# Optimization experiments

Hardware: AMD Instinct MI355X
Metric: run time of the kernel (lower is better)

## Reference

```python
import jax, jax.numpy as jnp
import numpy as np

B, N_COLS, N_PROMPTS, D = 1024, 256, 128, 256


def _ln(x, g, b, eps=1e-5):
    m = jnp.mean(x, axis=-1, keepdims=True)
    v = jnp.mean(jnp.square(x - m), axis=-1, keepdims=True)
    return (x - m) * jax.lax.rsqrt(v + eps) * g + b


def setup_inputs() -> dict:
    key = jax.random.key(0)
    ks = jax.random.split(key, 10)
    d_rs = D ** -0.5
    return {
        "x": jax.random.normal(ks[0], (B, N_COLS), jnp.float32),
        "prev_cell_out": jax.random.normal(ks[1], (B, N_PROMPTS, D), jnp.float32),
        "feature_emb_weight": jax.random.uniform(ks[2], (N_COLS, D), jnp.float32, -d_rs, d_rs),
        "feature_emb_bias": jax.random.uniform(ks[3], (N_COLS, D), jnp.float32, -d_rs, d_rs),
        "ln_emb_g": jnp.ones((D,), jnp.float32),
        "ln_emb_b": jnp.zeros((D,), jnp.float32),
        "ln_col_g": jnp.ones((D,), jnp.float32),
        "ln_col_b": jnp.zeros((D,), jnp.float32),
        "ln_prompt_g": jnp.ones((D,), jnp.float32),
        "ln_prompt_b": jnp.zeros((D,), jnp.float32),
        # torch Linear(2*D, D): weight [D, 2*D], y = x @ W^T + b
        "dense_imp_w": jax.random.normal(ks[4], (D, 2 * D), jnp.float32) * (2 * D) ** -0.5,
        "dense_imp_b": jnp.zeros((D,), jnp.float32),
        "emb_column": jax.random.normal(ks[5], (N_COLS, D), jnp.float32) * 0.01,
        "emb_prompt": jax.random.normal(ks[6], (N_PROMPTS, D), jnp.float32) * 0.01,
        # dense_expand = Linear(1, n_prompts): weight [n_prompts,1] squeezed -> [n_prompts]
        "expand_w": jax.random.normal(ks[7], (N_PROMPTS,), jnp.float32),
        "expand_b": jax.random.normal(ks[8], (N_PROMPTS,), jnp.float32) * 0.01,
    }


def reference(x, prev_cell_out, feature_emb_weight, feature_emb_bias,
              ln_emb_g, ln_emb_b, ln_col_g, ln_col_b, ln_prompt_g, ln_prompt_b,
              dense_imp_w, dense_imp_b, emb_column, emb_prompt,
              expand_w, expand_b):
    # feature embedding: [B, N, D]
    x_emb = jax.nn.relu(jnp.einsum('bn,nd->bnd', x, feature_emb_weight) + feature_emb_bias)
    x_emb = _ln(x_emb, ln_emb_g, ln_emb_b)
    # prompt update with residual
    xp = jnp.broadcast_to(emb_prompt[None], (x.shape[0], N_PROMPTS, D))  # [B, P, D]
    cat = jnp.concatenate([_ln(xp, ln_prompt_g, ln_prompt_b), prev_cell_out], axis=-1)  # [B, P, 2D]
    xp = jnp.einsum('bpk,dk->bpd', cat, dense_imp_w) + dense_imp_b + xp
    # column keys (shared across batch)
    col = _ln(emb_column, ln_col_g, ln_col_b)  # [N, D]
    mask = jax.nn.softmax(jnp.einsum('bpd,nd->bpn', xp, col), axis=-1)  # [B, P, N]
    V = jnp.einsum('bpn,bnd->bpd', mask, x_emb)  # [B, P, D]
    return V * (1.0 + expand_w)[None, :, None] + expand_b[None, :, None]
```

## Files before the change

kernel.cpp:

```cpp
#include <hip/hip_runtime.h>

#define NCOLS 256
#define NP    128
#define DD    256

typedef _Float16 half2 __attribute__((ext_vector_type(2)));
typedef _Float16 half4 __attribute__((ext_vector_type(4)));
typedef float    f32x4 __attribute__((ext_vector_type(4)));

#define MFMA16(a,b,c) __builtin_amdgcn_mfma_f32_16x16x16f16(a,b,c,0,0,0)

#define WS_COL_LN   0
#define WS_LNP      262144
#define WS_BASE     393216
#define WS_BLOG     524288
#define WS_CW16     655360
#define WS_WB16     786432

#define SMEM_LOGIT 67584
#define SMEM_PV    34816


__global__ __launch_bounds__(256) void k0a(
    const float* __restrict__ emb_column, const float* __restrict__ emb_prompt,
    const float* __restrict__ ln_col_g, const float* __restrict__ ln_col_b,
    const float* __restrict__ ln_prompt_g, const float* __restrict__ ln_prompt_b,
    const float* __restrict__ few, const float* __restrict__ feb,
    char* __restrict__ ws)
{
    __shared__ float red[10];
    int blk = blockIdx.x, tid = threadIdx.x;
    if (blk < 384) {
        const float *src, *g, *bb; float* dst;
        if (blk < 256) { int r = blk;     src = emb_column + r*DD; g = ln_col_g;    bb = ln_col_b;    dst = (float*)(ws + WS_COL_LN) + r*DD; }
        else           { int r = blk-256; src = emb_prompt + r*DD; g = ln_prompt_g; bb = ln_prompt_b; dst = (float*)(ws + WS_LNP) + r*DD; }
        float v = src[tid];
        float s = v, q = v*v;
        #pragma unroll
        for (int off = 32; off; off >>= 1) { s += __shfl_xor(s, off); q += __shfl_xor(q, off); }
        int wid = tid >> 6, lane = tid & 63;
        if (lane == 0) { red[wid] = s; red[4+wid] = q; }
        __syncthreads();
        if (tid == 0) {
            float S = red[0]+red[1]+red[2]+red[3];
            float Q = red[4]+red[5]+red[6]+red[7];
            float mu = S * (1.0f/DD);
            float var = Q * (1.0f/DD) - mu*mu;
            red[8] = mu; red[9] = rsqrtf(var + 1e-5f);
        }
        __syncthreads();
        dst[tid] = (v - red[8]) * red[9] * g[tid] + bb[tid];
    } else {
        int base = (blk - 384) * 512;
        half2* wb = (half2*)(ws + WS_WB16);
        #pragma unroll
        for (int j = 0; j < 2; ++j) {
            int idx = base + j*256 + tid;
            half2 h; h[0] = (_Float16)few[idx]; h[1] = (_Float16)feb[idx];
            wb[idx] = h;
        }
    }
}

__global__ __launch_bounds__(256) void k0b(
    const float* __restrict__ diw, const float* __restrict__ dib,
    const float* __restrict__ emb_prompt, char* __restrict__ ws)
{
    __shared__ float rowv[DD];
    int blk = blockIdx.x, tid = threadIdx.x;
    if (blk < 256) {
        int n = blk;
        const float* col_ln = (const float*)(ws + WS_COL_LN);
        rowv[tid] = col_ln[n*DD + tid];
        __syncthreads();
        float acc = 0.f;
        #pragma unroll 4
        for (int d = 0; d < DD; ++d) acc += rowv[d] * diw[d*512 + 256 + tid];
        int nt = n >> 4, lr = n & 15;
        int kc = tid >> 4, lq = (tid >> 2) & 3, j = tid & 3;
        ((_Float16*)(ws + WS_CW16))[((kc*16 + nt)*64 + lq*16 + lr)*4 + j] = (_Float16)acc;
    } else {
        int p = blk - 256;
        const float* lnp = (const float*)(ws + WS_LNP);
        rowv[tid] = lnp[p*DD + tid];
        __syncthreads();
        float acc = 0.f;
        #pragma unroll 4
        for (int k = 0; k < DD; ++k) acc += rowv[k] * diw[tid*512 + k];
        ((float*)(ws + WS_BASE))[p*DD + tid] = acc + dib[tid] + emb_prompt[p*DD + tid];
    }
}

__global__ __launch_bounds__(256) void k0c(char* __restrict__ ws)
{
    __shared__ float bs[DD];
    int p = blockIdx.x, n = threadIdx.x;
    const float* base   = (const float*)(ws + WS_BASE);
    const float* col_ln = (const float*)(ws + WS_COL_LN);
    bs[n] = base[p*DD + n];
    __syncthreads();
    float acc = 0.f;
    #pragma unroll 4
    for (int d = 0; d < DD; ++d) acc += bs[d] * col_ln[n*DD + d];
    ((float*)(ws + WS_BLOG))[p*DD + n] = acc;
}

__global__ __launch_bounds__(512, 4) void k_logit(
    const float* __restrict__ prev, const char* __restrict__ ws,
    char* __restrict__ pbuf)
{
    extern __shared__ char smem[];
    float* sm_m = (float*)(smem + 65536);
    float* sm_l = (float*)(smem + 66560);

    const char* cwbase = ws + WS_CW16;

    int bid = blockIdx.x;
    int b = bid >> 1, ph = bid & 1;
    int tid = threadIdx.x;
    int w = tid >> 6, l = tid & 63, lq = l >> 4, lr = l & 15;
    int pt = w >> 1, nh = w & 1;
    int pl = 16*pt + lr;
    int p  = 64*ph + pl;

    half4 pfrag[16];
    {
        const float* prow = prev + ((size_t)b*NP + p)*DD + 4*lq;
        #pragma unroll
        for (int kc = 0; kc < 16; ++kc) {
            f32x4 v = *(const f32x4*)(prow + 16*kc);
            half4 h;
            #pragma unroll
            for (int j = 0; j < 4; ++j) h[j] = (_Float16)v[j];
            pfrag[kc] = h;
        }
    }

    auto stage_cw = [&](int c, char* dst) {
        #pragma unroll
        for (int i = 0; i < 4; ++i) {
            int u = tid + 512*i;
            int kc = u >> 7, ntg = (u >> 5) & 3, rem = u & 31;
            uint4 v = *(const uint4*)(cwbase + kc*8192 + c*2048 + ntg*512 + rem*16);
            *(uint4*)(dst + u*16) = v;
        }
    };

    f32x4 acc[8];
    {
        const float* blrow = (const float*)(ws + WS_BLOG) + (size_t)p*DD + 4*lq;
        #pragma unroll
        for (int a = 0; a < 8; ++a)
            acc[a] = *(const f32x4*)(blrow + 16*(4*(a>>1) + 2*nh + (a&1)));
    }

    stage_cw(0, smem);
    __syncthreads();

    #pragma unroll
    for (int c = 0; c < 4; ++c) {
        char* cwc = smem + ((c & 1) ? 32768 : 0);
        char* cwn = smem + ((c & 1) ? 0 : 32768);

        uint4 st[4];
        if (c < 3) {
            #pragma unroll
            for (int i = 0; i < 4; ++i) {
                int u = tid + 512*i;
                int kc = u >> 7, ntg = (u >> 5) & 3, rem = u & 31;
                st[i] = *(const uint4*)(cwbase + kc*8192 + (c+1)*2048 + ntg*512 + rem*16);
            }
        }

        const char* cwl = cwc + l*8 + nh*1024;
        #pragma unroll
        for (int kc = 0; kc < 16; ++kc) {
            const char* fb = cwl + kc*2048;
            half4 a0 = *(const half4*)(fb);
            half4 a1 = *(const half4*)(fb + 512);
            half4 bp = pfrag[kc];
            acc[2*c]   = MFMA16(a0, bp, acc[2*c]);
            acc[2*c+1] = MFMA16(a1, bp, acc[2*c+1]);
        }

        if (c < 3) {
            #pragma unroll
            for (int i = 0; i < 4; ++i) {
                int u = tid + 512*i;
                *(uint4*)(cwn + u*16) = st[i];
            }
        }
        __syncthreads();
    }

    float pmax = -1e30f;
    #pragma unroll
    for (int a = 0; a < 8; ++a)
        #pragma unroll
        for (int r = 0; r < 4; ++r) pmax = fmaxf(pmax, acc[a][r]);
    pmax = fmaxf(pmax, __shfl_xor(pmax, 16));
    pmax = fmaxf(pmax, __shfl_xor(pmax, 32));
    if (lq == 0) sm_m[nh*64 + pl] = pmax;
    __syncthreads();
    float m = fmaxf(pmax, sm_m[(1 ^ nh)*64 + pl]);

    float s = 0.f;
    #pragma unroll
    for (int a = 0; a < 8; ++a)
        #pragma unroll
        for (int r = 0; r < 4; ++r) { float e = __expf(acc[a][r] - m); acc[a][r] = e; s += e; }
    s += __shfl_xor(s, 16);
    s += __shfl_xor(s, 32);
    if (lq == 0) sm_l[nh*64 + pl] = s;
    __syncthreads();
    float inv = 1.0f / (s + sm_l[(1 ^ nh)*64 + pl]);

    char* Pb = pbuf + (size_t)b*131072;
    #pragma unroll
    for (int a = 0; a < 8; ++a) {
        int NT = 4*(a >> 1) + 2*nh + (a & 1);
        half4 h;
        #pragma unroll
        for (int r = 0; r < 4; ++r) h[r] = (_Float16)(acc[a][r] * inv);
        *(half4*)(Pb + p*512 + NT*32 + lq*8) = h;
    }
}

__global__ __launch_bounds__(512, 4) void k_pv(
    const float* __restrict__ x,
    const float* __restrict__ expand_w, const float* __restrict__ expand_b,
    const float* __restrict__ ln_emb_g, const float* __restrict__ ln_emb_b,
    const char* __restrict__ ws, float* __restrict__ out)
{
    extern __shared__ char smem[];
    float* x_s = (float*)smem;
    char* xe0 = smem + 2048;
    char* xe1 = smem + 18432;

    const half2* WB = (const half2*)(ws + WS_WB16);

    int b = blockIdx.x;
    int tid = threadIdx.x;
    int w = tid >> 6, l = tid & 63, lq = l >> 4, lr = l & 15;
    int p = 16*w + lr;

    if (tid < 256) x_s[tid] = x[b*NCOLS + tid];
    float gcc[4], bcc[4];
    #pragma unroll
    for (int cc = 0; cc < 4; ++cc) {
        gcc[cc] = ln_emb_g[l + 64*cc];
        bcc[cc] = ln_emb_b[l + 64*cc];
    }

    const char* Pb = (const char*)out + (size_t)b*131072;

    auto compute_xe = [&](int c, char* xebuf) {
        int kc2 = w >> 2, lq2 = w & 3;
        float vj[4][4];
        #pragma unroll
        for (int j = 0; j < 4; ++j) {
            int n = c*32 + 16*kc2 + 4*lq2 + j;
            float xv = x_s[n];
            const half2* wbrow = WB + n*DD;
            float s = 0.f, q = 0.f;
            #pragma unroll
            for (int cc = 0; cc < 4; ++cc) {
                half2 pp = wbrow[l + 64*cc];
                float e = fmaf(xv, (float)pp[0], (float)pp[1]);
                e = e > 0.f ? e : 0.f;
                vj[j][cc] = e; s += e; q += e*e;
            }
            #pragma unroll
            for (int off = 32; off; off >>= 1) { s += __shfl_xor(s, off); q += __shfl_xor(q, off); }
            float mu = s * (1.0f/DD);
            float rs = rsqrtf(q*(1.0f/DD) - mu*mu + 1e-5f);
            #pragma unroll
            for (int cc = 0; cc < 4; ++cc)
                vj[j][cc] = (vj[j][cc]-mu)*rs*gcc[cc] + bcc[cc];
        }
        #pragma unroll
        for (int cc = 0; cc < 4; ++cc) {
            int dt = 4*cc + (l >> 4);
            half4 h;
            #pragma unroll
            for (int j = 0; j < 4; ++j) h[j] = (_Float16)vj[j][cc];
            *(half4*)(xebuf + (((kc2*16 + dt)*64) + lq2*16 + lr)*8) = h;
        }
    };

    __syncthreads();
    compute_xe(0, xe0);

    f32x4 acc_v[16];
    #pragma unroll
    for (int dt = 0; dt < 16; ++dt) acc_v[dt] = (f32x4){0.f,0.f,0.f,0.f};

    __syncthreads();

    for (int c = 0; c < 8; ++c) {
        char* xec = (c & 1) ? xe1 : xe0;
        char* xen = (c & 1) ? xe0 : xe1;

        half4 p16c[2];
        #pragma unroll
        for (int kc2 = 0; kc2 < 2; ++kc2)
            p16c[kc2] = *(const half4*)(Pb + p*512 + c*64 + kc2*32 + lq*8);

        if (c < 7) compute_xe(c+1, xen);

        const char* xel = xec + l*8;
        #pragma unroll
        for (int kc2 = 0; kc2 < 2; ++kc2) {
            half4 bp = p16c[kc2];
            const char* xb = xel + kc2*8192;
            #pragma unroll
            for (int dt = 0; dt < 16; ++dt) {
                half4 a = *(const half4*)(xb + dt*512);
                acc_v[dt] = MFMA16(a, bp, acc_v[dt]);
            }
        }

        __syncthreads();
    }

    {
        float sw = 1.0f + expand_w[p];
        float sb = expand_b[p];
        float* orow = out + ((size_t)b*NP + p)*DD + 4*lq;
        #pragma unroll
        for (int dt = 0; dt < 16; ++dt) {
            f32x4 v = acc_v[dt];
            #pragma unroll
            for (int r = 0; r < 4; ++r) v[r] = v[r]*sw + sb;
            *(f32x4*)(orow + 16*dt) = v;
        }
    }
}

extern "C" void kernel_launch(void* const* d_in, const int* in_sizes, int n_in,
                              void* d_out, int out_size, void* d_ws, size_t ws_size,
                              hipStream_t stream) {
    (void)in_sizes; (void)n_in; (void)out_size; (void)ws_size;
    const float* x           = (const float*)d_in[0];
    const float* prev        = (const float*)d_in[1];
    const float* few         = (const float*)d_in[2];
    const float* feb         = (const float*)d_in[3];
    const float* ln_emb_g    = (const float*)d_in[4];
    const float* ln_emb_b    = (const float*)d_in[5];
    const float* ln_col_g    = (const float*)d_in[6];
    const float* ln_col_b    = (const float*)d_in[7];
    const float* ln_prompt_g = (const float*)d_in[8];
    const float* ln_prompt_b = (const float*)d_in[9];
    const float* diw         = (const float*)d_in[10];
    const float* dib         = (const float*)d_in[11];
    const float* emb_column  = (const float*)d_in[12];
    const float* emb_prompt  = (const float*)d_in[13];
    const float* expand_w    = (const float*)d_in[14];
    const float* expand_b    = (const float*)d_in[15];
    char* ws = (char*)d_ws;
    float* out = (float*)d_out;

    k0a<<<512, 256, 0, stream>>>(emb_column, emb_prompt, ln_col_g, ln_col_b,
                                 ln_prompt_g, ln_prompt_b, few, feb, ws);
    k0b<<<384, 256, 0, stream>>>(diw, dib, emb_prompt, ws);
    k0c<<<128, 256, 0, stream>>>(ws);

    (void)hipFuncSetAttribute(reinterpret_cast<const void*>(k_logit),
                              hipFuncAttributeMaxDynamicSharedMemorySize, SMEM_LOGIT);
    k_logit<<<2048, 512, SMEM_LOGIT, stream>>>(prev, ws, (char*)d_out);

    (void)hipFuncSetAttribute(reinterpret_cast<const void*>(k_pv),
                              hipFuncAttributeMaxDynamicSharedMemorySize, SMEM_PV);
    k_pv<<<1024, 512, SMEM_PV, stream>>>(x, expand_w, expand_b,
                                         ln_emb_g, ln_emb_b, ws, out);
}
```

Measured before the change: 218.9 us.

## Fuse logit-softmax and PV kernels into one per-batch kernel with LDS-resident probabilities

Merges the logit/softmax kernel and the P·V kernel into a single 1024-thread block per batch element. The softmax probabilities stay in LDS with an XOR swizzle, so the fp16 P matrix no longer makes a round trip through global memory (the output buffer). The whole fp16 column-weight matrix is staged into LDS at once instead of being double-buffered in chunks. Each wave pair now splits the output D dimension, and the x_emb chunks are larger. The cost is about 131KB of LDS per block, which limits occupancy to roughly one block per CU, and fewer waves are available to hide latency.

```diff
diff --git a/kernel.cpp b/kernel.cpp
--- a/kernel.cpp
+++ b/kernel.cpp
@@ -17,8 +17,10 @@
 #define WS_CW16     655360
 #define WS_WB16     786432
 
-#define SMEM_LOGIT 67584
-#define SMEM_PV    34816
+#define LDS_CWP   3072
+#define LDS_XE0   68608
+#define LDS_XE1   101376
+#define SMEM_MAIN 134144
 
 
 __global__ __launch_bounds__(256) void k0a(
@@ -105,146 +107,103 @@
     ((float*)(ws + WS_BLOG))[p*DD + n] = acc;
 }
 
-__global__ __launch_bounds__(512, 4) void k_logit(
-    const float* __restrict__ prev, const char* __restrict__ ws,
-    char* __restrict__ pbuf)
-{
-    extern __shared__ char smem[];
-    float* sm_m = (float*)(smem + 65536);
-    float* sm_l = (float*)(smem + 66560);
-
-    const char* cwbase = ws + WS_CW16;
-
-    int bid = blockIdx.x;
-    int b = bid >> 1, ph = bid & 1;
-    int tid = threadIdx.x;
-    int w = tid >> 6, l = tid & 63, lq = l >> 4, lr = l & 15;
-    int pt = w >> 1, nh = w & 1;
-    int pl = 16*pt + lr;
-    int p  = 64*ph + pl;
-
-    half4 pfrag[16];
-    {
-        const float* prow = prev + ((size_t)b*NP + p)*DD + 4*lq;
-        #pragma unroll
-        for (int kc = 0; kc < 16; ++kc) {
-            f32x4 v = *(const f32x4*)(prow + 16*kc);
-            half4 h;
-            #pragma unroll
-            for (int j = 0; j < 4; ++j) h[j] = (_Float16)v[j];
-            pfrag[kc] = h;
-        }
-    }
-
-    auto stage_cw = [&](int c, char* dst) {
-        #pragma unroll
-        for (int i = 0; i < 4; ++i) {
-            int u = tid + 512*i;
-            int kc = u >> 7, ntg = (u >> 5) & 3, rem = u & 31;
-            uint4 v = *(const uint4*)(cwbase + kc*8192 + c*2048 + ntg*512 + rem*16);
-            *(uint4*)(dst + u*16) = v;
-        }
-    };
-
-    f32x4 acc[8];
-    {
-        const float* blrow = (const float*)(ws + WS_BLOG) + (size_t)p*DD + 4*lq;
-        #pragma unroll
-        for (int a = 0; a < 8; ++a)
-            acc[a] = *(const f32x4*)(blrow + 16*(4*(a>>1) + 2*nh + (a&1)));
-    }
-
-    stage_cw(0, smem);
-    __syncthreads();
-
-    #pragma unroll
-    for (int c = 0; c < 4; ++c) {
-        char* cwc = smem + ((c & 1) ? 32768 : 0);
-        char* cwn = smem + ((c & 1) ? 0 : 32768);
-
-        uint4 st[4];
-        if (c < 3) {
-            #pragma unroll
-            for (int i = 0; i < 4; ++i) {
-                int u = tid + 512*i;
-                int kc = u >> 7, ntg = (u >> 5) & 3, rem = u & 31;
-                st[i] = *(const uint4*)(cwbase + kc*8192 + (c+1)*2048 + ntg*512 + rem*16);
-            }
-        }
-
-        const char* cwl = cwc + l*8 + nh*1024;
-        #pragma unroll
-        for (int kc = 0; kc < 16; ++kc) {
-            const char* fb = cwl + kc*2048;
-            half4 a0 = *(const half4*)(fb);
-            half4 a1 = *(const half4*)(fb + 512);
-            half4 bp = pfrag[kc];
-            acc[2*c]   = MFMA16(a0, bp, acc[2*c]);
-            acc[2*c+1] = MFMA16(a1, bp, acc[2*c+1]);
-        }
-
-        if (c < 3) {
-            #pragma unroll
-            for (int i = 0; i < 4; ++i) {
-                int u = tid + 512*i;
-                *(uint4*)(cwn + u*16) = st[i];
-            }
-        }
-        __syncthreads();
-    }
-
-    float pmax = -1e30f;
-    #pragma unroll
-    for (int a = 0; a < 8; ++a)
-        #pragma unroll
-        for (int r = 0; r < 4; ++r) pmax = fmaxf(pmax, acc[a][r]);
-    pmax = fmaxf(pmax, __shfl_xor(pmax, 16));
-    pmax = fmaxf(pmax, __shfl_xor(pmax, 32));
-    if (lq == 0) sm_m[nh*64 + pl] = pmax;
-    __syncthreads();
-    float m = fmaxf(pmax, sm_m[(1 ^ nh)*64 + pl]);
-
-    float s = 0.f;
-    #pragma unroll
-    for (int a = 0; a < 8; ++a)
-        #pragma unroll
-        for (int r = 0; r < 4; ++r) { float e = __expf(acc[a][r] - m); acc[a][r] = e; s += e; }
-    s += __shfl_xor(s, 16);
-    s += __shfl_xor(s, 32);
-    if (lq == 0) sm_l[nh*64 + pl] = s;
-    __syncthreads();
-    float inv = 1.0f / (s + sm_l[(1 ^ nh)*64 + pl]);
-
-    char* Pb = pbuf + (size_t)b*131072;
-    #pragma unroll
-    for (int a = 0; a < 8; ++a) {
-        int NT = 4*(a >> 1) + 2*nh + (a & 1);
-        half4 h;
-        #pragma unroll
-        for (int r = 0; r < 4; ++r) h[r] = (_Float16)(acc[a][r] * inv);
-        *(half4*)(Pb + p*512 + NT*32 + lq*8) = h;
-    }
-}
-
-__global__ __launch_bounds__(512, 4) void k_pv(
-    const float* __restrict__ x,
+__global__ __launch_bounds__(1024) void trompt_main(
+    const float* __restrict__ x, const float* __restrict__ prev,
     const float* __restrict__ expand_w, const float* __restrict__ expand_b,
     const float* __restrict__ ln_emb_g, const float* __restrict__ ln_emb_b,
     const char* __restrict__ ws, float* __restrict__ out)
 {
     extern __shared__ char smem[];
-    float* x_s = (float*)smem;
-    char* xe0 = smem + 2048;
-    char* xe1 = smem + 18432;
-
-    const half2* WB = (const half2*)(ws + WS_WB16);
+    float* x_s  = (float*)(smem);
+    float* sm_m = (float*)(smem + 1024);
+    float* sm_l = (float*)(smem + 2048);
+    char*  cwP  = smem + LDS_CWP;
+    char*  xe0  = smem + LDS_XE0;
+    char*  xe1  = smem + LDS_XE1;
+
+    const char*  cwbase = ws + WS_CW16;
+    const half2* WB     = (const half2*)(ws + WS_WB16);
 
     int b = blockIdx.x;
     int tid = threadIdx.x;
     int w = tid >> 6, l = tid & 63, lq = l >> 4, lr = l & 15;
-    int p = 16*w + lr;
+    int pt = w >> 1, h = w & 1;
+    int p  = 16*pt + lr;
+    int pswz = (p & 7) << 4;
 
     if (tid < 256) x_s[tid] = x[b*NCOLS + tid];
+
+    #pragma unroll
+    for (int i = 0; i < 8; ++i) {
+        int u = tid + 1024*i;
+        *(uint4*)(cwP + u*16) = *(const uint4*)(cwbase + u*16);
+    }
+
+    half4 pfrag[16];
+    {
+        const float* prow = prev + ((size_t)b*NP + p)*DD + 4*lq;
+        #pragma unroll
+        for (int kc = 0; kc < 16; ++kc) {
+            f32x4 v = *(const f32x4*)(prow + 16*kc);
+            half4 hh;
+            #pragma unroll
+            for (int j = 0; j < 4; ++j) hh[j] = (_Float16)v[j];
+            pfrag[kc] = hh;
+        }
+    }
+
+    f32x4 acc[8];
+    {
+        const float* blrow = (const float*)(ws + WS_BLOG) + (size_t)p*DD + 4*lq;
+        #pragma unroll
+        for (int a = 0; a < 8; ++a) acc[a] = *(const f32x4*)(blrow + 16*(8*h + a));
+    }
+
+    __syncthreads();
+
+    {
+        const char* cwl = cwP + l*8 + (size_t)(8*h)*512;
+        #pragma unroll
+        for (int kc = 0; kc < 16; ++kc) {
+            const char* fb = cwl + (size_t)kc*8192;
+            half4 bp = pfrag[kc];
+            #pragma unroll
+            for (int a = 0; a < 8; ++a)
+                acc[a] = MFMA16(*(const half4*)(fb + a*512), bp, acc[a]);
+        }
+    }
+
+    float pmax = -1e30f;
+    #pragma unroll
+    for (int a = 0; a < 8; ++a)
+        #pragma unroll
+        for (int r = 0; r < 4; ++r) pmax = fmaxf(pmax, acc[a][r]);
+    pmax = fmaxf(pmax, __shfl_xor(pmax, 16));
+    pmax = fmaxf(pmax, __shfl_xor(pmax, 32));
+    if (lq == 0) sm_m[h*128 + p] = pmax;
+    __syncthreads();
+    float m = fmaxf(pmax, sm_m[(1 ^ h)*128 + p]);
+
+    float s = 0.f;
+    #pragma unroll
+    for (int a = 0; a < 8; ++a)
+        #pragma unroll
+        for (int r = 0; r < 4; ++r) { float e = __expf(acc[a][r] - m); acc[a][r] = e; s += e; }
+    s += __shfl_xor(s, 16);
+    s += __shfl_xor(s, 32);
+    if (lq == 0) sm_l[h*128 + p] = s;
+    __syncthreads();
+    float inv = 1.0f / (s + sm_l[(1 ^ h)*128 + p]);
+
+    #pragma unroll
+    for (int a = 0; a < 8; ++a) {
+        int nb = (8*h + a)*32 + lq*8;
+        half4 hh;
+        #pragma unroll
+        for (int r = 0; r < 4; ++r) hh[r] = (_Float16)(acc[a][r] * inv);
+        *(half4*)(cwP + p*512 + (nb ^ pswz)) = hh;
+    }
+
     float gcc[4], bcc[4];
     #pragma unroll
     for (int cc = 0; cc < 4; ++cc) {
@@ -252,28 +211,26 @@
         bcc[cc] = ln_emb_b[l + 64*cc];
     }
 
-    const char* Pb = (const char*)out + (size_t)b*131072;
-
     auto compute_xe = [&](int c, char* xebuf) {
-        int kc2 = w >> 2, lq2 = w & 3;
+        int kc2w = w >> 2, lq2 = w & 3;
         float vj[4][4];
         #pragma unroll
         for (int j = 0; j < 4; ++j) {
-            int n = c*32 + 16*kc2 + 4*lq2 + j;
+            int n = c*64 + 16*kc2w + 4*lq2 + j;
             float xv = x_s[n];
             const half2* wbrow = WB + n*DD;
-            float s = 0.f, q = 0.f;
+            float ss = 0.f, qq = 0.f;
             #pragma unroll
             for (int cc = 0; cc < 4; ++cc) {
                 half2 pp = wbrow[l + 64*cc];
                 float e = fmaf(xv, (float)pp[0], (float)pp[1]);
                 e = e > 0.f ? e : 0.f;
-                vj[j][cc] = e; s += e; q += e*e;
+                vj[j][cc] = e; ss += e; qq += e*e;
             }
             #pragma unroll
-            for (int off = 32; off; off >>= 1) { s += __shfl_xor(s, off); q += __shfl_xor(q, off); }
-            float mu = s * (1.0f/DD);
-            float rs = rsqrtf(q*(1.0f/DD) - mu*mu + 1e-5f);
+            for (int off = 32; off; off >>= 1) { ss += __shfl_xor(ss, off); qq += __shfl_xor(qq, off); }
+            float mu = ss * (1.0f/DD);
+            float rs = rsqrtf(qq*(1.0f/DD) - mu*mu + 1e-5f);
             #pragma unroll
             for (int cc = 0; cc < 4; ++cc)
                 vj[j][cc] = (vj[j][cc]-mu)*rs*gcc[cc] + bcc[cc];
@@ -281,58 +238,55 @@
         #pragma unroll
         for (int cc = 0; cc < 4; ++cc) {
             int dt = 4*cc + (l >> 4);
-            half4 h;
-            #pragma unroll
-            for (int j = 0; j < 4; ++j) h[j] = (_Float16)vj[j][cc];
-            *(half4*)(xebuf + (((kc2*16 + dt)*64) + lq2*16 + lr)*8) = h;
+            half4 hh;
+            #pragma unroll
+            for (int j = 0; j < 4; ++j) hh[j] = (_Float16)vj[j][cc];
+            *(half4*)(xebuf + (((kc2w*16 + dt)*64) + lq2*16 + lr)*8) = hh;
         }
     };
 
-    __syncthreads();
     compute_xe(0, xe0);
 
-    f32x4 acc_v[16];
-    #pragma unroll
-    for (int dt = 0; dt < 16; ++dt) acc_v[dt] = (f32x4){0.f,0.f,0.f,0.f};
-
-    __syncthreads();
-
-    for (int c = 0; c < 8; ++c) {
+    f32x4 acc_v[8];
+    #pragma unroll
+    for (int dtl = 0; dtl < 8; ++dtl) acc_v[dtl] = (f32x4){0.f,0.f,0.f,0.f};
+
+    __syncthreads();
+
+    for (int c = 0; c < 4; ++c) {
         char* xec = (c & 1) ? xe1 : xe0;
         char* xen = (c & 1) ? xe0 : xe1;
 
-        half4 p16c[2];
-        #pragma unroll
-        for (int kc2 = 0; kc2 < 2; ++kc2)
-            p16c[kc2] = *(const half4*)(Pb + p*512 + c*64 + kc2*32 + lq*8);
-
-        if (c < 7) compute_xe(c+1, xen);
+        half4 bp[4];
+        #pragma unroll
+        for (int kc2 = 0; kc2 < 4; ++kc2)
+            bp[kc2] = *(const half4*)(cwP + p*512 + ((c*128 + kc2*32 + lq*8) ^ pswz));
+
+        if (c < 3) compute_xe(c+1, xen);
 
         const char* xel = xec + l*8;
         #pragma unroll
-        for (int kc2 = 0; kc2 < 2; ++kc2) {
-            half4 bp = p16c[kc2];
-            const char* xb = xel + kc2*8192;
-            #pragma unroll
-            for (int dt = 0; dt < 16; ++dt) {
-                half4 a = *(const half4*)(xb + dt*512);
-                acc_v[dt] = MFMA16(a, bp, acc_v[dt]);
-            }
-        }
-
-        __syncthreads();
+        for (int kc2 = 0; kc2 < 4; ++kc2) {
+            const char* xb = xel + (size_t)(kc2*16 + 8*h)*512;
+            half4 bpc = bp[kc2];
+            #pragma unroll
+            for (int dtl = 0; dtl < 8; ++dtl)
+                acc_v[dtl] = MFMA16(*(const half4*)(xb + dtl*512), bpc, acc_v[dtl]);
+        }
+
+        if (c < 3) __syncthreads();
     }
 
     {
         float sw = 1.0f + expand_w[p];
         float sb = expand_b[p];
-        float* orow = out + ((size_t)b*NP + p)*DD + 4*lq;
-        #pragma unroll
-        for (int dt = 0; dt < 16; ++dt) {
-            f32x4 v = acc_v[dt];
+        float* orow = out + ((size_t)b*NP + p)*DD + 128*h + 4*lq;
+        #pragma unroll
+        for (int dtl = 0; dtl < 8; ++dtl) {
+            f32x4 v = acc_v[dtl];
             #pragma unroll
             for (int r = 0; r < 4; ++r) v[r] = v[r]*sw + sb;
-            *(f32x4*)(orow + 16*dt) = v;
+            *(f32x4*)(orow + 16*dtl) = v;
         }
     }
 }
@@ -365,12 +319,8 @@
     k0b<<<384, 256, 0, stream>>>(diw, dib, emb_prompt, ws);
     k0c<<<128, 256, 0, stream>>>(ws);
 
-    (void)hipFuncSetAttribute(reinterpret_cast<const void*>(k_logit),
-                              hipFuncAttributeMaxDynamicSharedMemorySize, SMEM_LOGIT);
-    k_logit<<<2048, 512, SMEM_LOGIT, stream>>>(prev, ws, (char*)d_out);
-
-    (void)hipFuncSetAttribute(reinterpret_cast<const void*>(k_pv),
-                              hipFuncAttributeMaxDynamicSharedMemorySize, SMEM_PV);
-    k_pv<<<1024, 512, SMEM_PV, stream>>>(x, expand_w, expand_b,
-                                         ln_emb_g, ln_emb_b, ws, out);
-}
+    (void)hipFuncSetAttribute(reinterpret_cast<const void*>(trompt_main),
+                              hipFuncAttributeMaxDynamicSharedMemorySize, SMEM_MAIN);
+    trompt_main<<<1024, 1024, SMEM_MAIN, stream>>>(x, prev, expand_w, expand_b,
+                                                   ln_emb_g, ln_emb_b, ws, out);
+}
```

Measured after the change: 195.5 us. 1.12x faster.
